# Kernel optimization log

Hardware: AMD Instinct MI355X
Metric: run time of the kernel (lower is better)

## Reference

```python
import jax, jax.numpy as jnp
import numpy as np

LMAX, MMAX, C = 4, 2, 128
E, N = 40000, 4000
CUTOFF, RESCALE = 12.0, 5.0
EPS = 1e-5

def _mappings(lmax, mmax):
    # l-major coefficient listing with m in [-min(l,mmax), min(l,mmax)]
    m_list = []
    for l in range(lmax + 1):
        mm = min(l, mmax)
        m_list += list(range(-mm, mm + 1))
    m_c = np.array(m_list)
    n = len(m_list)
    to_m = np.zeros((n, n), dtype=np.float32)  # m-major <- l-major permutation
    off = 0
    for m in range(mmax + 1):
        idx_r = np.where(m_c == m)[0]
        for i, j in enumerate(idx_r):
            to_m[off + i, j] = 1.0
        off += len(idx_r)
        if m > 0:
            idx_i = np.where(m_c == -m)[0]
            for i, j in enumerate(idx_i):
                to_m[off + i, j] = 1.0
            off += len(idx_i)
    full_m = np.concatenate([np.arange(-l, l + 1) for l in range(lmax + 1)])
    out_idx = np.where(np.abs(full_m) <= mmax)[0]  # out_mask as index list
    return jnp.asarray(to_m), jnp.asarray(out_idx)

TO_M, OUT_IDX = _mappings(LMAX, MMAX)
M0 = LMAX + 1            # number of m=0 coefficients (5)
M_ALL = TO_M.shape[0]    # number of |m|<=mmax coefficients (19)
NCOEF = (LMAX + 1) ** 2  # full coefficient count (25)

def setup_inputs() -> dict:
    key = jax.random.key(0)
    ks = jax.random.split(key, 8)
    return {
        "x": jax.random.normal(ks[0], (N, NCOEF, C), jnp.float32),
        "x_edge": jax.random.normal(ks[1], (E, 128), jnp.float32),
        "edge_distance": jax.random.uniform(ks[2], (E,), jnp.float32) * CUTOFF,
        "wigner_inv": jax.random.normal(ks[3], (E, NCOEF, NCOEF), jnp.float32) / np.float32(np.sqrt(NCOEF)),
        "edge_index": jax.random.randint(ks[4], (2, E), 0, N),
        "w1": jax.random.normal(ks[5], (128, 64), jnp.float32) / np.float32(np.sqrt(128.0)),
        "b1": jnp.zeros((64,), jnp.float32),
        "g1": jnp.ones((64,), jnp.float32),
        "be1": jnp.zeros((64,), jnp.float32),
        "w2": jax.random.normal(ks[6], (64, 64), jnp.float32) / 8.0,
        "b2": jnp.zeros((64,), jnp.float32),
        "g2": jnp.ones((64,), jnp.float32),
        "be2": jnp.zeros((64,), jnp.float32),
        "w3": jax.random.normal(ks[7], (64, M0 * C), jnp.float32) / 8.0,
        "b3": jnp.zeros((M0 * C,), jnp.float32),
        "node_offset": 0,
    }

def _ln(h, g, b):
    mu = jnp.mean(h, -1, keepdims=True)
    var = jnp.mean((h - mu) ** 2, -1, keepdims=True)
    return (h - mu) * jax.lax.rsqrt(var + EPS) * g + b

def _envelope(d):
    # PolynomialEnvelope with exponent p=5
    p = 5.0
    a = -(p + 1.0) * (p + 2.0) / 2.0   # -21
    bb = p * (p + 2.0)                 #  35
    c = -p * (p + 1.0) / 2.0           # -15
    env = 1.0 + a * d**5 + bb * d**6 + c * d**7
    return jnp.where(d < 1.0, env, jnp.zeros_like(d))

def reference(x, x_edge, edge_distance, wigner_inv, edge_index,
              w1, b1, g1, be1, w2, b2, g2, be2, w3, b3, node_offset):
    # RadialMLP: (Linear -> LayerNorm -> SiLU) x2 -> Linear
    h = jax.nn.silu(_ln(x_edge @ w1 + b1, g1, be1))
    h = jax.nn.silu(_ln(h @ w2 + b2, g2, be2))
    m0 = (h @ w3 + b3).reshape(-1, M0, C)               # [E, M0, C]
    # zero-padding to M_ALL rows then applying the permutation TO_M equals
    # contracting only the first M0 (m=0) rows of TO_M
    emb = jnp.einsum("nac,ab->nbc", m0, TO_M[:M0])       # [E, M_ALL, C] (l-order)
    emb = jnp.einsum("nij,njc->nic", wigner_inv[:, :, OUT_IDX], emb)  # [E, NCOEF, C]
    env = _envelope(edge_distance / CUTOFF)
    emb = emb * env[:, None, None]
    dst = edge_index[1] - node_offset
    return x.at[dst].add(emb / RESCALE)
```

## Files before the change

### kernel.cpp

```cpp
#include <hip/hip_runtime.h>
#include <cstddef>


constexpr int C_DIM   = 128;
constexpr int NCOEF   = 25;
constexpr int M0d     = 5;
constexpr int MCH     = 5;
constexpr float EPS_LN      = 1e-5f;
constexpr float INV_CUTOFF  = 1.0f / 12.0f;
constexpr float INV_RESCALE = 0.2f;

typedef __attribute__((ext_vector_type(8))) short short8;
typedef __attribute__((ext_vector_type(4))) short short4v;
typedef __attribute__((ext_vector_type(4))) float f32x4;

__device__ __forceinline__ short f2bf(float f) {
    unsigned u = __float_as_uint(f);
    unsigned r = u + 0x7FFFu + ((u >> 16) & 1u);
    return (short)(r >> 16);
}

__device__ __forceinline__ float silu(float z) {
    return z / (1.0f + __expf(-z));
}

__global__ __launch_bounds__(256) void prep_kernel(
    const float* __restrict__ w1, const float* __restrict__ w2,
    const float* __restrict__ w3,
    short* __restrict__ w1T, short* __restrict__ w2T, short* __restrict__ w3T,
    int* __restrict__ cnt, int n2)
{
    int i = blockIdx.x * 256 + threadIdx.x;
    if (i < n2) cnt[i] = 0;
    if (i < 64 * 128) {
        int n = i >> 7, k = i & 127;
        w1T[i] = f2bf(w1[k * 64 + n]);
    }
    if (i < 64 * 64) {
        int n = i >> 6, k = i & 63;
        w2T[i] = f2bf(w2[k * 64 + n]);
    }
    if (i < 640 * 64) {
        int n = i >> 6, k = i & 63;
        w3T[i] = f2bf(w3[k * 640 + n]);
    }
}

__global__ __launch_bounds__(256) void count_kernel(
    const int* __restrict__ edge_index, const int* __restrict__ noff,
    int* __restrict__ cnt, int E, int N)
{
    int e = blockIdx.x * 256 + threadIdx.x;
    if (e < E) {
        int d = edge_index[E + e] - noff[0];
        if (d >= 0 && d < N) atomicAdd(&cnt[d], 1);
    }
}

__global__ __launch_bounds__(256) void scan_kernel(
    const int* __restrict__ cnt, int* __restrict__ offs, int N)
{
    __shared__ int s_wsum[4];
    const int t = threadIdx.x;
    const int lane = t & 63, w = t >> 6;
    const int chunk = (N + 255) / 256;
    const int base = t * chunk;

    int s = 0;
    for (int j = 0; j < chunk; ++j)
        if (base + j < N) s += cnt[base + j];

    int v = s;
    #pragma unroll
    for (int off = 1; off < 64; off <<= 1) {
        int u = __shfl_up(v, off, 64);
        if (lane >= off) v += u;
    }
    if (lane == 63) s_wsum[w] = v;
    __syncthreads();
    int wbase = 0;
    for (int k = 0; k < w; ++k) wbase += s_wsum[k];
    int run = wbase + v - s;

    if (t == 0) offs[0] = 0;
    for (int j = 0; j < chunk; ++j) {
        if (base + j < N) {
            run += cnt[base + j];
            offs[base + j + 1] = run;
        }
    }
}

__global__ __launch_bounds__(256) void compact_kernel(
    const float* __restrict__ wigner_inv,
    const int*   __restrict__ edge_index,
    const int*   __restrict__ noff,
    const int*   __restrict__ offs,
    int*         __restrict__ cur,
    int*         __restrict__ ipos,
    unsigned short* __restrict__ wkT,
    int E, int N)
{
    __shared__ float s_raw[16 * 625];
    __shared__ int   s_ipos[16];

    const int t  = threadIdx.x;
    const int g0 = blockIdx.x * 16;
    const int nloc = (E - g0) < 16 ? (E - g0) : 16;

    if (t < nloc) {
        const int e = g0 + t;
        const int d = edge_index[E + e] - noff[0];
        int ip = -1;
        if (d >= 0 && d < N) {
            int p = atomicAdd(&cur[d], 1);
            ip = offs[d] + p;
        }
        s_ipos[t] = ip;
        ipos[e]   = ip;
    }

    if (nloc == 16) {
        const float4* src = (const float4*)(wigner_inv + (size_t)g0 * 625);
        #pragma unroll 4
        for (int f = t; f < 2500; f += 256)
            *(float4*)&s_raw[f * 4] = src[f];
    } else {
        const float* src = wigner_inv + (size_t)g0 * 625;
        for (int f = t; f < nloc * 625; f += 256)
            s_raw[f] = src[f];
    }
    __syncthreads();

    const int total = nloc * 160;
    #pragma unroll 4
    for (int f = t; f < total; f += 256) {
        int el = f / 160;
        int r  = f - el * 160;
        int a  = r >> 5;
        int i  = r & 31;
        int ip = s_ipos[el];
        if ((unsigned)ip < (unsigned)E) {
            unsigned short v = 0;
            if (i < 25) v = (unsigned short)f2bf(s_raw[el * 625 + i * 25 + a * (a + 1)]);
            wkT[((size_t)ip * 5 + a) * 32 + i] = v;
        }
    }
}

__global__ __launch_bounds__(256, 2) void mlp_mfma_kernel(
    const float* __restrict__ x_edge,
    const float* __restrict__ edge_distance,
    const int*   __restrict__ ipos,
    const short* __restrict__ w1T,
    const float* __restrict__ b1,
    const float* __restrict__ g1, const float* __restrict__ be1,
    const short* __restrict__ w2T,
    const float* __restrict__ b2,
    const float* __restrict__ g2, const float* __restrict__ be2,
    const short* __restrict__ w3T,
    const float* __restrict__ b3,
    unsigned short* __restrict__ m0p,
    int E, int nChunk)
{
    __shared__ float s_part[128];
    __shared__ short sh1[1024];
    __shared__ short sh2[1024];

    const int t   = threadIdx.x;
    const int w   = t >> 6;
    const int l   = t & 63;
    const int e16 = l & 15;
    const int g   = l >> 4;
    const int swz = (e16 & 7) << 4;

    char* sh1b = (char*)sh1;
    char* sh2b = (char*)sh2;

    short8 aw1[4], aw2[2], aw3a[10], aw3b[10];
    #pragma unroll
    for (int kt = 0; kt < 4; ++kt)
        aw1[kt] = *(const short8*)(w1T + (w * 16 + e16) * 128 + kt * 32 + 8 * g);
    #pragma unroll
    for (int kt = 0; kt < 2; ++kt)
        aw2[kt] = *(const short8*)(w2T + (w * 16 + e16) * 64 + kt * 32 + 8 * g);
    #pragma unroll
    for (int j = 0; j < 10; ++j) {
        const int nt = w * 10 + j;
        aw3a[j] = *(const short8*)(w3T + (nt * 16 + e16) * 64 + 8 * g);
        aw3b[j] = *(const short8*)(w3T + (nt * 16 + e16) * 64 + 32 + 8 * g);
    }
    const float4 b1v  = *(const float4*)(b1  + w * 16 + 4 * g);
    const float4 g1v  = *(const float4*)(g1  + w * 16 + 4 * g);
    const float4 be1v = *(const float4*)(be1 + w * 16 + 4 * g);
    const float4 b2v  = *(const float4*)(b2  + w * 16 + 4 * g);
    const float4 g2v  = *(const float4*)(g2  + w * 16 + 4 * g);
    const float4 be2v = *(const float4*)(be2 + w * 16 + 4 * g);
    float4 b3v[10];
    #pragma unroll
    for (int j = 0; j < 10; ++j)
        b3v[j] = *(const float4*)(b3 + (w * 10 + j) * 16 + 4 * g);

    const int ch0 = (int)blockIdx.x * MCH;
    const int chE = (ch0 + MCH < nChunk) ? (ch0 + MCH) : nChunk;

    for (int ch = ch0; ch < chE; ++ch) {
        const int g0  = ch * 16;
        const int row = g0 + e16;
        const int rowc = row < E ? row : (E - 1);
        const bool valid = row < E;

        float sc;
        {
            float d  = edge_distance[rowc] * INV_CUTOFF;
            float d2 = d * d;
            float d5 = d2 * d2 * d;
            float env = 1.0f + d5 * (-21.0f + d * (35.0f + d * (-15.0f)));
            sc = ((d < 1.0f) ? env : 0.0f) * INV_RESCALE;
        }
        const int ip = valid ? ipos[rowc] : -1;
        const bool ipok = valid && ((unsigned)ip < (unsigned)E);

        short8 bx[4];
        {
            const float* xr = x_edge + (size_t)rowc * C_DIM + 8 * g;
            #pragma unroll
            for (int kt = 0; kt < 4; ++kt) {
                float4 f0 = *(const float4*)(xr + kt * 32);
                float4 f1 = *(const float4*)(xr + kt * 32 + 4);
                short8 v;
                v[0] = f2bf(f0.x); v[1] = f2bf(f0.y); v[2] = f2bf(f0.z); v[3] = f2bf(f0.w);
                v[4] = f2bf(f1.x); v[5] = f2bf(f1.y); v[6] = f2bf(f1.z); v[7] = f2bf(f1.w);
                bx[kt] = v;
            }
        }

        f32x4 acc1 = {b1v.x, b1v.y, b1v.z, b1v.w};
        #pragma unroll
        for (int kt = 0; kt < 4; ++kt)
            acc1 = __builtin_amdgcn_mfma_f32_16x16x32_bf16(aw1[kt], bx[kt], acc1, 0, 0, 0);

        {
            float s = acc1[0] + acc1[1] + acc1[2] + acc1[3];
            float qq = acc1[0]*acc1[0] + acc1[1]*acc1[1] + acc1[2]*acc1[2] + acc1[3]*acc1[3];
            s  += __shfl_xor(s, 16);  s  += __shfl_xor(s, 32);
            qq += __shfl_xor(qq, 16); qq += __shfl_xor(qq, 32);
            if (g == 0) { s_part[w * 16 + e16] = s; s_part[64 + w * 16 + e16] = qq; }
            __syncthreads();
            float mu  = (s_part[e16] + s_part[16 + e16] + s_part[32 + e16] + s_part[48 + e16])
                        * (1.0f / 64.0f);
            float ex2 = (s_part[64 + e16] + s_part[80 + e16] + s_part[96 + e16] + s_part[112 + e16])
                        * (1.0f / 64.0f);
            float var = ex2 - mu * mu;
            float rstd = rsqrtf((var > 0.0f ? var : 0.0f) + EPS_LN);
            short4v hv;
            hv[0] = f2bf(silu((acc1[0] - mu) * rstd * g1v.x + be1v.x));
            hv[1] = f2bf(silu((acc1[1] - mu) * rstd * g1v.y + be1v.y));
            hv[2] = f2bf(silu((acc1[2] - mu) * rstd * g1v.z + be1v.z));
            hv[3] = f2bf(silu((acc1[3] - mu) * rstd * g1v.w + be1v.w));
            __syncthreads();
            *(short4v*)(sh1b + e16 * 128 + ((w * 32 + 8 * g) ^ swz)) = hv;
            __syncthreads();
        }

        f32x4 acc2 = {b2v.x, b2v.y, b2v.z, b2v.w};
        {
            short8 bh[2];
            #pragma unroll
            for (int kt = 0; kt < 2; ++kt)
                bh[kt] = *(const short8*)(sh1b + e16 * 128 + ((kt * 64 + 16 * g) ^ swz));
            #pragma unroll
            for (int kt = 0; kt < 2; ++kt)
                acc2 = __builtin_amdgcn_mfma_f32_16x16x32_bf16(aw2[kt], bh[kt], acc2, 0, 0, 0);
        }

        {
            float s = acc2[0] + acc2[1] + acc2[2] + acc2[3];
            float qq = acc2[0]*acc2[0] + acc2[1]*acc2[1] + acc2[2]*acc2[2] + acc2[3]*acc2[3];
            s  += __shfl_xor(s, 16);  s  += __shfl_xor(s, 32);
            qq += __shfl_xor(qq, 16); qq += __shfl_xor(qq, 32);
            if (g == 0) { s_part[w * 16 + e16] = s; s_part[64 + w * 16 + e16] = qq; }
            __syncthreads();
            float mu  = (s_part[e16] + s_part[16 + e16] + s_part[32 + e16] + s_part[48 + e16])
                        * (1.0f / 64.0f);
            float ex2 = (s_part[64 + e16] + s_part[80 + e16] + s_part[96 + e16] + s_part[112 + e16])
                        * (1.0f / 64.0f);
            float var = ex2 - mu * mu;
            float rstd = rsqrtf((var > 0.0f ? var : 0.0f) + EPS_LN);
            short4v hv;
            hv[0] = f2bf(silu((acc2[0] - mu) * rstd * g2v.x + be2v.x));
            hv[1] = f2bf(silu((acc2[1] - mu) * rstd * g2v.y + be2v.y));
            hv[2] = f2bf(silu((acc2[2] - mu) * rstd * g2v.z + be2v.z));
            hv[3] = f2bf(silu((acc2[3] - mu) * rstd * g2v.w + be2v.w));
            __syncthreads();
            *(short4v*)(sh2b + e16 * 128 + ((w * 32 + 8 * g) ^ swz)) = hv;
            __syncthreads();
        }

        {
            short8 bh2[2];
            #pragma unroll
            for (int kt = 0; kt < 2; ++kt)
                bh2[kt] = *(const short8*)(sh2b + e16 * 128 + ((kt * 64 + 16 * g) ^ swz));

            #pragma unroll
            for (int j = 0; j < 10; ++j) {
                const int nt = w * 10 + j;
                f32x4 a3 = {b3v[j].x, b3v[j].y, b3v[j].z, b3v[j].w};
                a3 = __builtin_amdgcn_mfma_f32_16x16x32_bf16(aw3a[j], bh2[0], a3, 0, 0, 0);
                a3 = __builtin_amdgcn_mfma_f32_16x16x32_bf16(aw3b[j], bh2[1], a3, 0, 0, 0);
                if (ipok) {
                    short4v o;
                    o[0] = f2bf(a3[0] * sc);
                    o[1] = f2bf(a3[1] * sc);
                    o[2] = f2bf(a3[2] * sc);
                    o[3] = f2bf(a3[3] * sc);
                    *(short4v*)(m0p + ((size_t)ip * 5 + (nt >> 3)) * 128
                                    + ((nt & 7) << 4) + 4 * g) = o;
                }
            }
        }
        __syncthreads();
    }
}

__global__ __launch_bounds__(256, 4) void gather_mfma_kernel(
    const float* __restrict__ x,
    const unsigned short* __restrict__ m0p,
    const unsigned short* __restrict__ wkT,
    const int* __restrict__ offs,
    float* __restrict__ out, int N)
{
    const int n  = blockIdx.x;
    const int t  = threadIdx.x;
    const int w  = t >> 6;
    const int l  = t & 63;
    const int ln = l & 15;
    const int q  = l >> 4;
    const int myk = 8 * q;

    const int beg = offs[n], end = offs[n + 1];
    const int K = 5 * (end - beg);
    const size_t beg5 = (size_t)5 * beg;
    const size_t obase = (size_t)n * (NCOEF * C_DIM);

    float xv[2][4][2];
    #pragma unroll
    for (int mt = 0; mt < 2; ++mt) {
        #pragma unroll
        for (int r = 0; r < 4; ++r) {
            const int i = mt * 16 + 4 * q + r;
            #pragma unroll
            for (int bt = 0; bt < 2; ++bt)
                xv[mt][r][bt] = (i < NCOEF)
                    ? x[obase + (size_t)i * C_DIM + 32 * w + bt * 16 + ln] : 0.0f;
        }
    }

    f32x4 acc[2][2];
    #pragma unroll
    for (int mt = 0; mt < 2; ++mt)
        #pragma unroll
        for (int bt = 0; bt < 2; ++bt)
            acc[mt][bt] = (f32x4){0.f, 0.f, 0.f, 0.f};

    const int nk = (K + 31) >> 5;

#define LOADF(KT, AF, BF) do {                                                  \
    const int kb_ = (KT) * 32;                                                  \
    const unsigned short* wrow_ = wkT + (beg5 + kb_ + myk) * 32 + ln;           \
    const unsigned short* mrow_ = m0p + (beg5 + kb_ + myk) * 128 + w * 32 + ln; \
    if (kb_ + 32 <= K) {                                                        \
        _Pragma("unroll")                                                       \
        for (int j = 0; j < 8; ++j) {                                           \
            AF[0][j] = (short)wrow_[j * 32];                                    \
            AF[1][j] = (short)wrow_[j * 32 + 16];                               \
            BF[0][j] = (short)mrow_[j * 128];                                   \
            BF[1][j] = (short)mrow_[j * 128 + 16];                              \
        }                                                                       \
    } else {                                                                    \
        const int limit_ = K - kb_;                                             \
        _Pragma("unroll")                                                       \
        for (int j = 0; j < 8; ++j) {                                           \
            const bool ok_ = (myk + j) < limit_;                                \
            AF[0][j] = ok_ ? (short)wrow_[j * 32] : (short)0;                   \
            AF[1][j] = ok_ ? (short)wrow_[j * 32 + 16] : (short)0;              \
            BF[0][j] = ok_ ? (short)mrow_[j * 128] : (short)0;                  \
            BF[1][j] = ok_ ? (short)mrow_[j * 128 + 16] : (short)0;             \
        }                                                                       \
    } } while (0)

#define MFMA4(AF, BF) do {                                                              \
    acc[0][0] = __builtin_amdgcn_mfma_f32_16x16x32_bf16(AF[0], BF[0], acc[0][0], 0,0,0);\
    acc[0][1] = __builtin_amdgcn_mfma_f32_16x16x32_bf16(AF[0], BF[1], acc[0][1], 0,0,0);\
    acc[1][0] = __builtin_amdgcn_mfma_f32_16x16x32_bf16(AF[1], BF[0], acc[1][0], 0,0,0);\
    acc[1][1] = __builtin_amdgcn_mfma_f32_16x16x32_bf16(AF[1], BF[1], acc[1][1], 0,0,0);\
    } while (0)

    short8 afA[2], bfA[2], afB[2], bfB[2];
    if (nk > 0) {
        LOADF(0, afA, bfA);
        int kt = 0;
        while (true) {
            if (kt + 1 < nk) LOADF(kt + 1, afB, bfB);
            MFMA4(afA, bfA);
            ++kt;
            if (kt >= nk) break;
            if (kt + 1 < nk) LOADF(kt + 1, afA, bfA);
            MFMA4(afB, bfB);
            ++kt;
            if (kt >= nk) break;
        }
    }
#undef LOADF
#undef MFMA4

    #pragma unroll
    for (int mt = 0; mt < 2; ++mt) {
        #pragma unroll
        for (int r = 0; r < 4; ++r) {
            const int i = mt * 16 + 4 * q + r;
            if (i < NCOEF) {
                #pragma unroll
                for (int bt = 0; bt < 2; ++bt) {
                    const size_t idx = obase + (size_t)i * C_DIM + 32 * w + bt * 16 + ln;
                    out[idx] = xv[mt][r][bt] + acc[mt][bt][r];
                }
            }
        }
    }
}

constexpr int FEB = 8;
constexpr int BT  = 256;

__device__ __forceinline__ float ln_silu(float v, float g, float be) {
    float s = v;
    #pragma unroll
    for (int o = 32; o; o >>= 1) s += __shfl_xor(s, o, 64);
    float mu = s * (1.0f / 64.0f);
    float dv = v - mu;
    float q  = dv * dv;
    #pragma unroll
    for (int o = 32; o; o >>= 1) q += __shfl_xor(q, o, 64);
    float rstd = rsqrtf(q * (1.0f / 64.0f) + EPS_LN);
    float z = dv * rstd * g + be;
    return z / (1.0f + __expf(-z));
}

__global__ __launch_bounds__(BT) void edge_degree_fallback(
    const float* __restrict__ x_edge, const float* __restrict__ edge_distance,
    const float* __restrict__ wigner_inv, const int* __restrict__ edge_index,
    const float* __restrict__ w1, const float* __restrict__ b1,
    const float* __restrict__ g1, const float* __restrict__ be1,
    const float* __restrict__ w2, const float* __restrict__ b2,
    const float* __restrict__ g2, const float* __restrict__ be2,
    const float* __restrict__ w3, const float* __restrict__ b3,
    const int* __restrict__ node_offset_p, float* __restrict__ out, int E)
{
    __shared__ float s_xe[FEB][C_DIM];
    __shared__ float s_h1[FEB][64];
    __shared__ float s_h2[FEB][64];
    __shared__ float s_wig[FEB][NCOEF * M0d];
    __shared__ float s_scale[FEB];
    __shared__ int   s_dst[FEB];

    const int t = threadIdx.x;
    const int g0 = blockIdx.x * FEB;
    const int ne = (E - g0) < FEB ? (E - g0) : FEB;

    {
        const float* src = x_edge + (size_t)g0 * C_DIM;
        for (int f = t; f < FEB * C_DIM; f += BT) {
            int e = f >> 7;
            ((float*)s_xe)[f] = (e < ne) ? src[f] : 0.0f;
        }
    }
    {
        const int wcol_[M0d] = {0, 2, 6, 12, 20};
        for (int f = t; f < FEB * NCOEF * M0d; f += BT) {
            int e = f / 125, r = f - e * 125, i = r / 5, a = r - i * 5;
            float v = 0.0f;
            if (e < ne)
                v = wigner_inv[((size_t)(g0 + e)) * (NCOEF * NCOEF) + i * NCOEF + wcol_[a]];
            s_wig[e][r] = v;
        }
    }
    if (t < FEB) {
        if (t < ne) {
            float d = edge_distance[g0 + t] * INV_CUTOFF;
            float d2 = d * d, d5 = d2 * d2 * d;
            float env = 1.0f + d5 * (-21.0f + d * (35.0f + d * (-15.0f)));
            s_scale[t] = ((d < 1.0f) ? env : 0.0f) * INV_RESCALE;
            s_dst[t] = edge_index[E + g0 + t] - node_offset_p[0];
        } else { s_scale[t] = 0.0f; s_dst[t] = 0; }
    }
    __syncthreads();

    const int wv = t >> 6, j = t & 63;
    {
        float acc0 = b1[j], acc1 = acc0;
        for (int k = 0; k < C_DIM; ++k) {
            float w = w1[k * 64 + j];
            acc0 += s_xe[wv][k] * w;
            acc1 += s_xe[wv + 4][k] * w;
        }
        const float g = g1[j], be = be1[j];
        s_h1[wv][j]     = ln_silu(acc0, g, be);
        s_h1[wv + 4][j] = ln_silu(acc1, g, be);
    }
    __syncthreads();
    {
        float acc0 = b2[j], acc1 = acc0;
        for (int k = 0; k < 64; ++k) {
            float w = w2[k * 64 + j];
            acc0 += s_h1[wv][k] * w;
            acc1 += s_h1[wv + 4][k] * w;
        }
        const float g = g2[j], be = be2[j];
        s_h2[wv][j]     = ln_silu(acc0, g, be);
        s_h2[wv + 4][j] = ln_silu(acc1, g, be);
    }
    __syncthreads();

    const int c = t & 127, half = t >> 7;
    float m0r[4][M0d];
    #pragma unroll
    for (int a = 0; a < M0d; ++a) {
        float bb = b3[a * C_DIM + c];
        float a0 = bb, a1 = bb, a2 = bb, a3 = bb;
        const float* w3c = w3 + a * C_DIM + c;
        for (int k = 0; k < 64; ++k) {
            float w = w3c[k * (M0d * C_DIM)];
            a0 += s_h2[half + 0][k] * w;
            a1 += s_h2[half + 2][k] * w;
            a2 += s_h2[half + 4][k] * w;
            a3 += s_h2[half + 6][k] * w;
        }
        m0r[0][a] = a0; m0r[1][a] = a1; m0r[2][a] = a2; m0r[3][a] = a3;
    }
    #pragma unroll
    for (int ei = 0; ei < 4; ++ei) {
        const int e = half + 2 * ei;
        if (e >= ne) continue;
        const float sc = s_scale[e];
        float* obase = out + (size_t)s_dst[e] * (NCOEF * C_DIM) + c;
        #pragma unroll
        for (int i = 0; i < NCOEF; ++i) {
            const float* wg = &s_wig[e][i * M0d];
            float v = wg[0] * m0r[ei][0] + wg[1] * m0r[ei][1] + wg[2] * m0r[ei][2]
                    + wg[3] * m0r[ei][3] + wg[4] * m0r[ei][4];
            atomicAdd(obase + i * C_DIM, v * sc);
        }
    }
}

extern "C" void kernel_launch(void* const* d_in, const int* in_sizes, int n_in,
                              void* d_out, int out_size, void* d_ws, size_t ws_size,
                              hipStream_t stream)
{
    const float* x             = (const float*)d_in[0];
    const float* x_edge        = (const float*)d_in[1];
    const float* edge_distance = (const float*)d_in[2];
    const float* wigner_inv    = (const float*)d_in[3];
    const int*   edge_index    = (const int*)d_in[4];
    const float* w1  = (const float*)d_in[5];
    const float* b1  = (const float*)d_in[6];
    const float* g1  = (const float*)d_in[7];
    const float* be1 = (const float*)d_in[8];
    const float* w2  = (const float*)d_in[9];
    const float* b2  = (const float*)d_in[10];
    const float* g2  = (const float*)d_in[11];
    const float* be2 = (const float*)d_in[12];
    const float* w3  = (const float*)d_in[13];
    const float* b3  = (const float*)d_in[14];
    const int*   node_offset = (const int*)d_in[15];

    float* out = (float*)d_out;
    const int E = in_sizes[1] / C_DIM;
    const int N = in_sizes[0] / (NCOEF * C_DIM);
    const size_t KROWS = (size_t)5 * E + 32;

    size_t off = 0;
    const size_t m0p_off  = off; off += KROWS * 128 * 2;
    const size_t wkT_off  = off; off += KROWS * 32 * 2;
    const size_t cnt_off  = off; off += (size_t)N * 4;
    const size_t cur_off  = off; off += (size_t)N * 4;
    const size_t offs_off = off; off += (size_t)(N + 1) * 4;
    const size_t ipos_off = off; off += (size_t)E * 4;
    off = (off + 255) & ~(size_t)255;
    const size_t w1T_off  = off; off += 64 * 128 * 2;
    const size_t w2T_off  = off; off += 64 * 64 * 2;
    const size_t w3T_off  = off; off += 640 * 64 * 2;
    const size_t need     = off;

    if (ws_size >= need) {
        char* ws   = (char*)d_ws;
        unsigned short* m0p = (unsigned short*)(ws + m0p_off);
        unsigned short* wkT = (unsigned short*)(ws + wkT_off);
        int* cnt   = (int*)(ws + cnt_off);
        int* cur   = (int*)(ws + cur_off);
        int* offs  = (int*)(ws + offs_off);
        int* ipos  = (int*)(ws + ipos_off);
        short* w1T = (short*)(ws + w1T_off);
        short* w2T = (short*)(ws + w2T_off);
        short* w3T = (short*)(ws + w3T_off);

        const int prepN = (640 * 64 > 2 * N) ? 640 * 64 : 2 * N;
        prep_kernel<<<(prepN + 255) / 256, 256, 0, stream>>>(
            w1, w2, w3, w1T, w2T, w3T, cnt, 2 * N);
        count_kernel<<<(E + 255) / 256, 256, 0, stream>>>(edge_index, node_offset, cnt, E, N);
        scan_kernel<<<1, 256, 0, stream>>>(cnt, offs, N);

        compact_kernel<<<(E + 15) / 16, 256, 0, stream>>>(
            wigner_inv, edge_index, node_offset, offs, cur, ipos, wkT, E, N);

        const int nChunk = (E + 15) / 16;
        mlp_mfma_kernel<<<(nChunk + MCH - 1) / MCH, 256, 0, stream>>>(
            x_edge, edge_distance, ipos,
            w1T, b1, g1, be1, w2T, b2, g2, be2, w3T, b3, m0p, E, nChunk);

        gather_mfma_kernel<<<N, 256, 0, stream>>>(x, m0p, wkT, offs, out, N);
    } else {
        hipMemcpyAsync(out, x, (size_t)out_size * sizeof(float),
                       hipMemcpyDeviceToDevice, stream);
        edge_degree_fallback<<<(E + FEB - 1) / FEB, BT, 0, stream>>>(
            x_edge, edge_distance, wigner_inv, edge_index,
            w1, b1, g1, be1, w2, b2, g2, be2, w3, b3,
            node_offset, out, E);
    }
}
```

Measured before the change: 113.2 us.

## Fuse wigner compaction and slot assignment into the MLP kernel

Removes the separate compact kernel and performs per-edge slot assignment (atomic on per-node cursor) and the bf16 transposed wigner extraction inside the MLP kernel, chunk by chunk. This drops one kernel launch and the ipos array round trip through global memory. In exchange the MLP kernel stages 8 edges of wigner data at a time through a 20KB shared buffer with extra barriers per chunk. That larger shared footprint and the added serialization may hurt occupancy and overlap with the MFMA work.

```diff
diff --git a/kernel.cpp b/kernel.cpp
--- a/kernel.cpp
+++ b/kernel.cpp
@@ -91,67 +91,14 @@
     }
 }
 
-__global__ __launch_bounds__(256) void compact_kernel(
+__global__ __launch_bounds__(256, 2) void mlp_mfma_kernel(
+    const float* __restrict__ x_edge,
+    const float* __restrict__ edge_distance,
     const float* __restrict__ wigner_inv,
     const int*   __restrict__ edge_index,
     const int*   __restrict__ noff,
     const int*   __restrict__ offs,
     int*         __restrict__ cur,
-    int*         __restrict__ ipos,
-    unsigned short* __restrict__ wkT,
-    int E, int N)
-{
-    __shared__ float s_raw[16 * 625];
-    __shared__ int   s_ipos[16];
-
-    const int t  = threadIdx.x;
-    const int g0 = blockIdx.x * 16;
-    const int nloc = (E - g0) < 16 ? (E - g0) : 16;
-
-    if (t < nloc) {
-        const int e = g0 + t;
-        const int d = edge_index[E + e] - noff[0];
-        int ip = -1;
-        if (d >= 0 && d < N) {
-            int p = atomicAdd(&cur[d], 1);
-            ip = offs[d] + p;
-        }
-        s_ipos[t] = ip;
-        ipos[e]   = ip;
-    }
-
-    if (nloc == 16) {
-        const float4* src = (const float4*)(wigner_inv + (size_t)g0 * 625);
-        #pragma unroll 4
-        for (int f = t; f < 2500; f += 256)
-            *(float4*)&s_raw[f * 4] = src[f];
-    } else {
-        const float* src = wigner_inv + (size_t)g0 * 625;
-        for (int f = t; f < nloc * 625; f += 256)
-            s_raw[f] = src[f];
-    }
-    __syncthreads();
-
-    const int total = nloc * 160;
-    #pragma unroll 4
-    for (int f = t; f < total; f += 256) {
-        int el = f / 160;
-        int r  = f - el * 160;
-        int a  = r >> 5;
-        int i  = r & 31;
-        int ip = s_ipos[el];
-        if ((unsigned)ip < (unsigned)E) {
-            unsigned short v = 0;
-            if (i < 25) v = (unsigned short)f2bf(s_raw[el * 625 + i * 25 + a * (a + 1)]);
-            wkT[((size_t)ip * 5 + a) * 32 + i] = v;
-        }
-    }
-}
-
-__global__ __launch_bounds__(256, 2) void mlp_mfma_kernel(
-    const float* __restrict__ x_edge,
-    const float* __restrict__ edge_distance,
-    const int*   __restrict__ ipos,
     const short* __restrict__ w1T,
     const float* __restrict__ b1,
     const float* __restrict__ g1, const float* __restrict__ be1,
@@ -161,11 +108,14 @@
     const short* __restrict__ w3T,
     const float* __restrict__ b3,
     unsigned short* __restrict__ m0p,
-    int E, int nChunk)
+    unsigned short* __restrict__ wkT,
+    int E, int N, int nChunk)
 {
+    __shared__ __align__(16) float s_wig[8 * 625];
     __shared__ float s_part[128];
     __shared__ short sh1[1024];
     __shared__ short sh2[1024];
+    __shared__ int   s_ip[16];
 
     const int t   = threadIdx.x;
     const int w   = t >> 6;
@@ -210,6 +160,54 @@
         const int rowc = row < E ? row : (E - 1);
         const bool valid = row < E;
 
+        if (t < 16) {
+            const int e = g0 + t;
+            int ip = -1;
+            if (e < E) {
+                const int d = edge_index[E + e] - noff[0];
+                if (d >= 0 && d < N) {
+                    int p = atomicAdd(&cur[d], 1);
+                    ip = offs[d] + p;
+                }
+            }
+            s_ip[t] = ip;
+        }
+        __syncthreads();
+
+        #pragma unroll
+        for (int h = 0; h < 2; ++h) {
+            const int e0 = g0 + 8 * h;
+            const int nh = (E - e0) < 8 ? ((E - e0) < 0 ? 0 : (E - e0)) : 8;
+            if (nh == 8) {
+                const float4* src = (const float4*)(wigner_inv + (size_t)e0 * 625);
+                #pragma unroll 5
+                for (int f = t; f < 1250; f += 256)
+                    ((float4*)s_wig)[f] = src[f];
+            } else if (nh > 0) {
+                const float* src = wigner_inv + (size_t)e0 * 625;
+                for (int f = t; f < nh * 625; f += 256)
+                    s_wig[f] = src[f];
+            }
+            __syncthreads();
+            if (nh > 0) {
+                const int total = nh * 160;
+                #pragma unroll 2
+                for (int f = t; f < total; f += 256) {
+                    const int el = f / 160;
+                    const int r  = f - el * 160;
+                    const int a  = r >> 5;
+                    const int i  = r & 31;
+                    const int ip = s_ip[8 * h + el];
+                    if ((unsigned)ip < (unsigned)E) {
+                        unsigned short v = 0;
+                        if (i < 25) v = (unsigned short)f2bf(s_wig[el * 625 + i * 25 + a * (a + 1)]);
+                        wkT[((size_t)ip * 5 + a) * 32 + i] = v;
+                    }
+                }
+            }
+            __syncthreads();
+        }
+
         float sc;
         {
             float d  = edge_distance[rowc] * INV_CUTOFF;
@@ -218,7 +216,7 @@
             float env = 1.0f + d5 * (-21.0f + d * (35.0f + d * (-15.0f)));
             sc = ((d < 1.0f) ? env : 0.0f) * INV_RESCALE;
         }
-        const int ip = valid ? ipos[rowc] : -1;
+        const int ip = valid ? s_ip[e16] : -1;
         const bool ipok = valid && ((unsigned)ip < (unsigned)E);
 
         short8 bx[4];
@@ -587,7 +585,6 @@
     const size_t cnt_off  = off; off += (size_t)N * 4;
     const size_t cur_off  = off; off += (size_t)N * 4;
     const size_t offs_off = off; off += (size_t)(N + 1) * 4;
-    const size_t ipos_off = off; off += (size_t)E * 4;
     off = (off + 255) & ~(size_t)255;
     const size_t w1T_off  = off; off += 64 * 128 * 2;
     const size_t w2T_off  = off; off += 64 * 64 * 2;
@@ -601,7 +598,6 @@
         int* cnt   = (int*)(ws + cnt_off);
         int* cur   = (int*)(ws + cur_off);
         int* offs  = (int*)(ws + offs_off);
-        int* ipos  = (int*)(ws + ipos_off);
         short* w1T = (short*)(ws + w1T_off);
         short* w2T = (short*)(ws + w2T_off);
         short* w3T = (short*)(ws + w3T_off);
@@ -612,13 +608,10 @@
         count_kernel<<<(E + 255) / 256, 256, 0, stream>>>(edge_index, node_offset, cnt, E, N);
         scan_kernel<<<1, 256, 0, stream>>>(cnt, offs, N);
 
-        compact_kernel<<<(E + 15) / 16, 256, 0, stream>>>(
-            wigner_inv, edge_index, node_offset, offs, cur, ipos, wkT, E, N);
-
         const int nChunk = (E + 15) / 16;
         mlp_mfma_kernel<<<(nChunk + MCH - 1) / MCH, 256, 0, stream>>>(
-            x_edge, edge_distance, ipos,
-            w1T, b1, g1, be1, w2T, b2, g2, be2, w3T, b3, m0p, E, nChunk);
+            x_edge, edge_distance, wigner_inv, edge_index, node_offset, offs, cur,
+            w1T, b1, g1, be1, w2T, b2, g2, be2, w3T, b3, m0p, wkT, E, N, nChunk);
 
         gather_mfma_kernel<<<N, 256, 0, stream>>>(x, m0p, wkT, offs, out, N);
     } else {
```

Result: slower. 147.6 us (+30.5%).
